# Optimization experiments

Hardware: AMD Instinct MI355X
Metric: run time of the kernel (lower is better)

Reference implementation:

```python
import jax, jax.numpy as jnp
import numpy as np

N_PTS = 131072
K_POSE = 4
J = 24
P_NUM = 64
R_COMP = 32
POSE_DIM = 32
GRID = (512, 512, 128)
MAT_MODE = ((0, 1), (0, 2), (1, 2))


def sample_line(line, xs):
    # line: [k, R, G], xs: [N] in [-1, 1].
    # Equivalent to F.grid_sample on a [k,R,G,1] map with grid x-coord fixed to 0
    # (W==1 so the x dim is degenerate) -> 1D linear interpolation along G.
    G = line.shape[-1]
    pos = (xs + 1.0) * 0.5 * (G - 1)
    i0 = jnp.clip(jnp.floor(pos), 0, G - 1).astype(jnp.int32)
    i1 = jnp.clip(i0 + 1, 0, G - 1)
    w = pos - i0.astype(xs.dtype)
    v0 = jnp.take(line, i0, axis=-1)  # [k,R,N]
    v1 = jnp.take(line, i1, axis=-1)
    return v0 * (1.0 - w) + v1 * w


def blend(w, A):
    # w: [1,N,J], A: [1,J,4,4] -> per-point blended LBS transform [1,N,4,4]
    return jnp.einsum('bnj,bjuv->bnuv', w, A)


def lbs_points(pts, T, inverse):
    Rm = T[..., :3, :3]
    t = T[..., :3, 3]
    if inverse:
        return jnp.einsum('bnij,bnj->bni', jnp.linalg.inv(Rm), pts - t)
    return jnp.einsum('bnij,bnj->bni', Rm, pts) + t


def lbs_dirs(d, T, inverse):
    Rm = T[..., :3, :3]
    if inverse:
        return jnp.einsum('bnij,bnj->bni', jnp.linalg.inv(Rm), d)
    return jnp.einsum('bnij,bnj->bni', Rm, d)


def setup_inputs() -> dict:
    key = jax.random.key(0)
    ks = jax.random.split(key, 12)
    pose_pts = 0.3 * jax.random.normal(ks[0], (1, N_PTS, 3), jnp.float32)
    pose_dirs = jax.random.normal(ks[1], (1, N_PTS, 3), jnp.float32)
    sw = jax.random.uniform(ks[2], (1, N_PTS, J), dtype=jnp.float32)
    skinning_weight = sw / jnp.sum(sw, axis=-1, keepdims=True)
    eye = jnp.eye(4, dtype=jnp.float32)
    A = eye + 0.2 * jax.random.normal(ks[3], (1, J, 4, 4), jnp.float32)
    big_A = eye + 0.2 * jax.random.normal(ks[4], (1, J, 4, 4), jnp.float32)
    tbounds = jnp.array([[-1.5, -1.5, -1.5], [1.5, 1.5, 1.5]], jnp.float32)
    coord_line0 = 0.1 * jax.random.normal(ks[5], (P_NUM, R_COMP, GRID[0], 1), jnp.float32)
    coord_line1 = 0.1 * jax.random.normal(ks[6], (P_NUM, R_COMP, GRID[1], 1), jnp.float32)
    coord_line2 = 0.1 * jax.random.normal(ks[7], (P_NUM, R_COMP, GRID[2], 1), jnp.float32)
    feat_line0 = 0.1 * jax.random.normal(ks[8], (P_NUM, R_COMP, POSE_DIM, 1), jnp.float32)
    feat_line1 = 0.1 * jax.random.normal(ks[9], (P_NUM, R_COMP, POSE_DIM, 1), jnp.float32)
    feat_line2 = 0.1 * jax.random.normal(ks[10], (P_NUM, R_COMP, POSE_DIM, 1), jnp.float32)
    tw = jax.random.uniform(ks[11], (K_POSE,), dtype=jnp.float32) + 0.1
    topk_weight = tw / jnp.sum(tw)  # L1-normalized top-k pose weights
    topk_id = jax.random.randint(jax.random.fold_in(key, 7), (K_POSE,), 0, P_NUM, dtype=jnp.int32)
    return dict(pose_pts=pose_pts, pose_dirs=pose_dirs, skinning_weight=skinning_weight,
                A=A, big_A=big_A, tbounds=tbounds,
                coord_line0=coord_line0, coord_line1=coord_line1, coord_line2=coord_line2,
                feat_line0=feat_line0, feat_line1=feat_line1, feat_line2=feat_line2,
                topk_weight=topk_weight, topk_id=topk_id)


def reference(pose_pts, pose_dirs, skinning_weight, A, big_A, tbounds,
              coord_line0, coord_line1, coord_line2,
              feat_line0, feat_line1, feat_line2,
              topk_weight, topk_id):
    # --- backward_deform: observed pose -> t-pose (inv A) -> big/canonical pose (big_A) ---
    T_A = blend(skinning_weight, A)
    T_big = blend(skinning_weight, big_A)
    tpose = lbs_points(pose_pts, T_A, inverse=True)
    cnl_pts = lbs_points(tpose, T_big, inverse=False)   # [1,N,3]
    tdirs = lbs_dirs(pose_dirs, T_A, inverse=True)
    cnl_dirs = lbs_dirs(tdirs, T_big, inverse=False)    # [1,N,3]
    # --- get_pose_feat: normalize_pts detaches pts, then TensoRF-style line sampling ---
    npts = jax.lax.stop_gradient(cnl_pts)
    npts = (npts - tbounds[0]) / (tbounds[1] - tbounds[0]) * 2.0 - 1.0  # [1,N,3]
    coord_lines = (coord_line0, coord_line1, coord_line2)
    feat_lines = (feat_line0, feat_line1, feat_line2)
    coords, feats = [], []
    for i in range(3):
        line = coord_lines[i][topk_id][..., 0]           # [k,R,G_i]
        coords.append(sample_line(line, npts[0, :, i]))  # [k,R,N]
        feats.append(feat_lines[i][topk_id][..., 0])     # [k,R,C]
    planes = []
    for p, (i0, i1) in enumerate(MAT_MODE):
        t = coords[i0] * coords[i1]                      # [k,R,N] outer-product term
        planes.append(jnp.einsum('krn,krc->knc', t, feats[p]))  # reduce over R
    pose_feats = jnp.concatenate(planes, axis=-1)        # [k,N,3C]
    pose_feat = jnp.sum(topk_weight[:, None, None] * pose_feats, axis=0, keepdims=True)
    return jnp.concatenate([cnl_pts, cnl_dirs, pose_feat], axis=-1)  # [1,N,102]
```

## Files before the change

kernel.cpp:

```cpp
#include <hip/hip_runtime.h>

#define NPTS 131072
#define G0 512
#define G1 512
#define G2 128

#define SKIN_BLOCKS  512
#define TRANS_BLOCKS 576
#define FEAT_BLOCKS  48

#define OFF1 (4*G0*32)
#define OFF2 (4*(G0+G1)*32)
#define LTOT (4*(G0+G1+G2)*32)

typedef float v4f __attribute__((ext_vector_type(4)));
typedef __attribute__((ext_vector_type(8))) short short8;

__device__ unsigned short g_lines16[LTOT + 32];
__device__ unsigned short g_featB[3*4*2*64*8];
__device__ float4 g_pos[NPTS];

__device__ __forceinline__ unsigned short bf16rne(float x){
  unsigned int u = __float_as_uint(x);
  u += 0x7fffu + ((u >> 16) & 1u);
  return (unsigned short)(u >> 16);
}

__device__ __forceinline__ void cvt8(uint4 r, float* f){
  f[0] = __uint_as_float(r.x << 16); f[1] = __uint_as_float(r.x & 0xffff0000u);
  f[2] = __uint_as_float(r.y << 16); f[3] = __uint_as_float(r.y & 0xffff0000u);
  f[4] = __uint_as_float(r.z << 16); f[5] = __uint_as_float(r.z & 0xffff0000u);
  f[6] = __uint_as_float(r.w << 16); f[7] = __uint_as_float(r.w & 0xffff0000u);
}

__device__ __forceinline__ void lerp_rows(const unsigned short* p, float w, float* c){
  uint4 r0 = *(const uint4*)p;
  uint4 r1 = *(const uint4*)(p + 32);
  float a[8], b[8];
  cvt8(r0, a); cvt8(r1, b);
  #pragma unroll
  for (int j = 0; j < 8; j++) c[j] = fmaf(w, b[j] - a[j], a[j]);
}

__device__ __forceinline__ unsigned int pack2(float lo, float hi){
  unsigned int ul = __float_as_uint(lo) + 0x8000u;
  unsigned int uh = __float_as_uint(hi) + 0x8000u;
  return __builtin_amdgcn_perm(uh, ul, 0x07060302u);
}

__global__ __launch_bounds__(256) void prep_skin(
    const float* __restrict__ pts, const float* __restrict__ dirs,
    const float* __restrict__ sw,  const float* __restrict__ Am,
    const float* __restrict__ Bm,  const float* __restrict__ tb,
    const float* __restrict__ c0,  const float* __restrict__ c1,
    const float* __restrict__ c2,  const float* __restrict__ f0,
    const float* __restrict__ f1,  const float* __restrict__ f2,
    const float* __restrict__ tw,  const int* __restrict__ topk_id,
    float* __restrict__ out)
{
  const int bid = blockIdx.x;
  const int tid = threadIdx.x;

  if (bid >= SKIN_BLOCKS) {
    int pb = bid - SKIN_BLOCKS;
    if (pb < TRANS_BLOCKS) {
      int e = pb*256 + tid;
      const float* src; int logG, outoff;
      if (e < 65536)       { src = c0; logG = 9; outoff = 0; }
      else if (e < 131072) { e -= 65536;  src = c1; logG = 9; outoff = OFF1; }
      else                 { e -= 131072; src = c2; logG = 7; outoff = OFF2; }
      const int G = 1 << logG;
      int g  = e & (G-1);
      int t  = e >> logG;
      int r  = t & 31;
      int kk = t >> 5;
      int id = topk_id[kk];
      float v = src[(id*32 + r)*G + g];
      g_lines16[outoff + (kk*G + g)*32 + r] = bf16rne(v);
    } else {
      int e = (pb - TRANS_BLOCKS)*256 + tid;
      if (e < 3*4*2*64*8) {
        int j    =  e        & 7;
        int lane = (e >> 3)  & 63;
        int tcol = (e >> 9)  & 1;
        int s    = (e >> 10) & 3;
        int p    =  e >> 12;
        int r = ((lane >> 4) << 3) + j;
        int cc = tcol*16 + (lane & 15);
        const float* f = (p == 0) ? f0 : ((p == 1) ? f1 : f2);
        float v = tw[s] * f[(topk_id[s]*32 + r)*32 + cc];
        g_featB[e] = bf16rne(v);
      }
    }
    return;
  }

  if (bid == 0 && tid < 32) g_lines16[LTOT + tid] = 0;

  __shared__ float sA[384];
  __shared__ float sB[384];
  for (int i = tid; i < 384; i += 256){ sA[i] = Am[i]; sB[i] = Bm[i]; }
  __syncthreads();

  const int n = bid*256 + tid;
  float swv[24];
  {
    const float4* swp = reinterpret_cast<const float4*>(sw + n*24);
    #pragma unroll
    for (int i = 0; i < 6; i++){
      float4 v = swp[i];
      swv[4*i] = v.x; swv[4*i+1] = v.y; swv[4*i+2] = v.z; swv[4*i+3] = v.w;
    }
  }
  float RA[9] = {0,0,0,0,0,0,0,0,0}, tA[3] = {0,0,0};
  float RB[9] = {0,0,0,0,0,0,0,0,0}, tB[3] = {0,0,0};
  #pragma unroll
  for (int j = 0; j < 24; j++){
    float w = swv[j];
    const float* a = sA + j*16;
    const float* b = sB + j*16;
    RA[0] = fmaf(w, a[0], RA[0]); RA[1] = fmaf(w, a[1], RA[1]); RA[2] = fmaf(w, a[2], RA[2]); tA[0] = fmaf(w, a[3],  tA[0]);
    RA[3] = fmaf(w, a[4], RA[3]); RA[4] = fmaf(w, a[5], RA[4]); RA[5] = fmaf(w, a[6], RA[5]); tA[1] = fmaf(w, a[7],  tA[1]);
    RA[6] = fmaf(w, a[8], RA[6]); RA[7] = fmaf(w, a[9], RA[7]); RA[8] = fmaf(w, a[10],RA[8]); tA[2] = fmaf(w, a[11], tA[2]);
    RB[0] = fmaf(w, b[0], RB[0]); RB[1] = fmaf(w, b[1], RB[1]); RB[2] = fmaf(w, b[2], RB[2]); tB[0] = fmaf(w, b[3],  tB[0]);
    RB[3] = fmaf(w, b[4], RB[3]); RB[4] = fmaf(w, b[5], RB[4]); RB[5] = fmaf(w, b[6], RB[5]); tB[1] = fmaf(w, b[7],  tB[1]);
    RB[6] = fmaf(w, b[8], RB[6]); RB[7] = fmaf(w, b[9], RB[7]); RB[8] = fmaf(w, b[10],RB[8]); tB[2] = fmaf(w, b[11], tB[2]);
  }
  float c00 = RA[4]*RA[8] - RA[5]*RA[7];
  float c01 = RA[5]*RA[6] - RA[3]*RA[8];
  float c02 = RA[3]*RA[7] - RA[4]*RA[6];
  float det = RA[0]*c00 + RA[1]*c01 + RA[2]*c02;
  float idet = 1.0f/det;
  float i00 = c00*idet;
  float i01 = (RA[2]*RA[7] - RA[1]*RA[8])*idet;
  float i02 = (RA[1]*RA[5] - RA[2]*RA[4])*idet;
  float i10 = c01*idet;
  float i11 = (RA[0]*RA[8] - RA[2]*RA[6])*idet;
  float i12 = (RA[2]*RA[3] - RA[0]*RA[5])*idet;
  float i20 = c02*idet;
  float i21 = (RA[1]*RA[6] - RA[0]*RA[7])*idet;
  float i22 = (RA[0]*RA[4] - RA[1]*RA[3])*idet;

  float px = pts[n*3+0], py = pts[n*3+1], pz = pts[n*3+2];
  float dx = dirs[n*3+0], dy = dirs[n*3+1], dz = dirs[n*3+2];
  float qx = px - tA[0], qy = py - tA[1], qz = pz - tA[2];
  float tpx = i00*qx + i01*qy + i02*qz;
  float tpy = i10*qx + i11*qy + i12*qz;
  float tpz = i20*qx + i21*qy + i22*qz;
  float cx = RB[0]*tpx + RB[1]*tpy + RB[2]*tpz + tB[0];
  float cy = RB[3]*tpx + RB[4]*tpy + RB[5]*tpz + tB[1];
  float cz = RB[6]*tpx + RB[7]*tpy + RB[8]*tpz + tB[2];
  float tdx = i00*dx + i01*dy + i02*dz;
  float tdy = i10*dx + i11*dy + i12*dz;
  float tdz = i20*dx + i21*dy + i22*dz;
  float cdx = RB[0]*tdx + RB[1]*tdy + RB[2]*tdz;
  float cdy = RB[3]*tdx + RB[4]*tdy + RB[5]*tdz;
  float cdz = RB[6]*tdx + RB[7]*tdy + RB[8]*tdz;

  {
    float* o = out + (size_t)n*102;
    o[0] = cx; o[1] = cy; o[2] = cz; o[3] = cdx; o[4] = cdy; o[5] = cdz;
  }
  {
    float lo0 = tb[0], lo1 = tb[1], lo2 = tb[2];
    float hi0 = tb[3], hi1 = tb[4], hi2 = tb[5];
    float x0 = (cx - lo0)/(hi0 - lo0)*2.0f - 1.0f;
    float x1 = (cy - lo1)/(hi1 - lo1)*2.0f - 1.0f;
    float x2 = (cz - lo2)/(hi2 - lo2)*2.0f - 1.0f;
    float4 p;
    p.x = (x0 + 1.0f)*0.5f*(float)(G0-1);
    p.y = (x1 + 1.0f)*0.5f*(float)(G1-1);
    p.z = (x2 + 1.0f)*0.5f*(float)(G2-1);
    p.w = 0.0f;
    g_pos[n] = p;
  }
}

__global__ __launch_bounds__(256) void einsum_mfma(float* __restrict__ out)
{
  const int tid  = threadIdx.x;
  const int lane = tid & 63;
  const int wv   = tid >> 6;
  const int m    = lane & 15;
  const int q    = lane >> 4;
  const int tile = blockIdx.x*4 + wv;
  const int pl   = tile*16 + m;

  float4 pos = g_pos[pl];
  float pc0 = fminf(fmaxf(pos.x, 0.0f), (float)(G0-1));
  float pc1 = fminf(fmaxf(pos.y, 0.0f), (float)(G1-1));
  float pc2 = fminf(fmaxf(pos.z, 0.0f), (float)(G2-1));
  float fl0 = floorf(pc0), fl1 = floorf(pc1), fl2 = floorf(pc2);
  int a0 = (int)fl0, a1 = (int)fl1, a2 = (int)fl2;
  float w0 = pc0 - fl0, w1 = pc1 - fl1, w2 = pc2 - fl2;

  const unsigned short* lt0 = g_lines16;
  const unsigned short* lt1 = g_lines16 + OFF1;
  const unsigned short* lt2 = g_lines16 + OFF2;
  const short8* fb = reinterpret_cast<const short8*>(g_featB);

  v4f acc00 = {0,0,0,0}, acc01 = {0,0,0,0};
  v4f acc10 = {0,0,0,0}, acc11 = {0,0,0,0};
  v4f acc20 = {0,0,0,0}, acc21 = {0,0,0,0};

  #pragma unroll
  for (int s = 0; s < 4; s++){
    float c0[8], c1[8], c2[8];
    lerp_rows(lt0 + (s*G0 + a0)*32 + q*8, w0, c0);
    lerp_rows(lt1 + (s*G1 + a1)*32 + q*8, w1, c1);
    lerp_rows(lt2 + (s*G2 + a2)*32 + q*8, w2, c2);

    uint4 A0u, A1u, A2u;
    A0u.x = pack2(c0[0]*c1[0], c0[1]*c1[1]);
    A0u.y = pack2(c0[2]*c1[2], c0[3]*c1[3]);
    A0u.z = pack2(c0[4]*c1[4], c0[5]*c1[5]);
    A0u.w = pack2(c0[6]*c1[6], c0[7]*c1[7]);
    A1u.x = pack2(c0[0]*c2[0], c0[1]*c2[1]);
    A1u.y = pack2(c0[2]*c2[2], c0[3]*c2[3]);
    A1u.z = pack2(c0[4]*c2[4], c0[5]*c2[5]);
    A1u.w = pack2(c0[6]*c2[6], c0[7]*c2[7]);
    A2u.x = pack2(c1[0]*c2[0], c1[1]*c2[1]);
    A2u.y = pack2(c1[2]*c2[2], c1[3]*c2[3]);
    A2u.z = pack2(c1[4]*c2[4], c1[5]*c2[5]);
    A2u.w = pack2(c1[6]*c2[6], c1[7]*c2[7]);
    short8 A0 = __builtin_bit_cast(short8, A0u);
    short8 A1 = __builtin_bit_cast(short8, A1u);
    short8 A2 = __builtin_bit_cast(short8, A2u);

    short8 B00 = fb[(0*8 + s*2 + 0)*64 + lane];
    short8 B01 = fb[(0*8 + s*2 + 1)*64 + lane];
    short8 B10 = fb[(1*8 + s*2 + 0)*64 + lane];
    short8 B11 = fb[(1*8 + s*2 + 1)*64 + lane];
    short8 B20 = fb[(2*8 + s*2 + 0)*64 + lane];
    short8 B21 = fb[(2*8 + s*2 + 1)*64 + lane];
    acc00 = __builtin_amdgcn_mfma_f32_16x16x32_bf16(A0, B00, acc00, 0, 0, 0);
    acc01 = __builtin_amdgcn_mfma_f32_16x16x32_bf16(A0, B01, acc01, 0, 0, 0);
    acc10 = __builtin_amdgcn_mfma_f32_16x16x32_bf16(A1, B10, acc10, 0, 0, 0);
    acc11 = __builtin_amdgcn_mfma_f32_16x16x32_bf16(A1, B11, acc11, 0, 0, 0);
    acc20 = __builtin_amdgcn_mfma_f32_16x16x32_bf16(A2, B20, acc20, 0, 0, 0);
    acc21 = __builtin_amdgcn_mfma_f32_16x16x32_bf16(A2, B21, acc21, 0, 0, 0);
  }

  const int rowBase = tile*16 + q*4;
  #pragma unroll
  for (int v = 0; v < 4; v++){
    float* o = out + (size_t)(rowBase + v)*102 + 6 + m;
    o[0]  = acc00[v];
    o[16] = acc01[v];
    o[32] = acc10[v];
    o[48] = acc11[v];
    o[64] = acc20[v];
    o[80] = acc21[v];
  }
}

extern "C" void kernel_launch(void* const* d_in, const int* in_sizes, int n_in,
                              void* d_out, int out_size, void* d_ws, size_t ws_size,
                              hipStream_t stream) {
  const float* pose_pts  = (const float*)d_in[0];
  const float* pose_dirs = (const float*)d_in[1];
  const float* sw        = (const float*)d_in[2];
  const float* Am        = (const float*)d_in[3];
  const float* Bm        = (const float*)d_in[4];
  const float* tb        = (const float*)d_in[5];
  const float* cl0       = (const float*)d_in[6];
  const float* cl1       = (const float*)d_in[7];
  const float* cl2       = (const float*)d_in[8];
  const float* fl0       = (const float*)d_in[9];
  const float* fl1       = (const float*)d_in[10];
  const float* fl2       = (const float*)d_in[11];
  const float* tw        = (const float*)d_in[12];
  const int*   tkid      = (const int*)d_in[13];
  float* out = (float*)d_out;

  hipLaunchKernelGGL(prep_skin, dim3(SKIN_BLOCKS + TRANS_BLOCKS + FEAT_BLOCKS), dim3(256), 0, stream,
                     pose_pts, pose_dirs, sw, Am, Bm, tb,
                     cl0, cl1, cl2, fl0, fl1, fl2, tw, tkid, out);
  hipLaunchKernelGGL(einsum_mfma, dim3(NPTS/(4*16)), dim3(256), 0, stream, out);
}
```

Before: 137.0 us.

## Process two point tiles per wave, vectorize line transpose and skin output stores

The einsum kernel now handles two 16-point tiles per wave. It issues all six gathered line-row loads for both tiles before the lerp and MFMA work, and reuses each B fragment load across both tiles, which halves the grid. The line transpose in the prep kernel now packs four bf16 values per thread into an 8-byte store, cutting its block count by four. The six leading output floats are written as three float2 stores. The cost is higher register pressure from twelve accumulators and buffered loads, which may reduce occupancy.

```diff
diff --git a/kernel.cpp b/kernel.cpp
--- a/kernel.cpp
+++ b/kernel.cpp
@@ -6,7 +6,7 @@
 #define G2 128
 
 #define SKIN_BLOCKS  512
-#define TRANS_BLOCKS 576
+#define TRANS_BLOCKS 144
 #define FEAT_BLOCKS  48
 
 #define OFF1 (4*G0*32)
@@ -33,9 +33,7 @@
   f[6] = __uint_as_float(r.w << 16); f[7] = __uint_as_float(r.w & 0xffff0000u);
 }
 
-__device__ __forceinline__ void lerp_rows(const unsigned short* p, float w, float* c){
-  uint4 r0 = *(const uint4*)p;
-  uint4 r1 = *(const uint4*)(p + 32);
+__device__ __forceinline__ void lerp_regs(uint4 r0, uint4 r1, float w, float* c){
   float a[8], b[8];
   cvt8(r0, a); cvt8(r1, b);
   #pragma unroll
@@ -66,17 +64,24 @@
     if (pb < TRANS_BLOCKS) {
       int e = pb*256 + tid;
       const float* src; int logG, outoff;
-      if (e < 65536)       { src = c0; logG = 9; outoff = 0; }
-      else if (e < 131072) { e -= 65536;  src = c1; logG = 9; outoff = OFF1; }
-      else                 { e -= 131072; src = c2; logG = 7; outoff = OFF2; }
+      if (e < 16384)      { src = c0; logG = 9; outoff = 0; }
+      else if (e < 32768) { e -= 16384; src = c1; logG = 9; outoff = OFF1; }
+      else                { e -= 32768; src = c2; logG = 7; outoff = OFF2; }
       const int G = 1 << logG;
       int g  = e & (G-1);
       int t  = e >> logG;
-      int r  = t & 31;
-      int kk = t >> 5;
+      int r4 = t & 7;
+      int kk = t >> 3;
       int id = topk_id[kk];
-      float v = src[(id*32 + r)*G + g];
-      g_lines16[outoff + (kk*G + g)*32 + r] = bf16rne(v);
+      const float* s0 = src + (id*32 + r4*4)*G + g;
+      float v0 = s0[0];
+      float v1 = s0[G];
+      float v2 = s0[2*G];
+      float v3 = s0[3*G];
+      unsigned int lo = ((unsigned int)bf16rne(v0)) | (((unsigned int)bf16rne(v1)) << 16);
+      unsigned int hi = ((unsigned int)bf16rne(v2)) | (((unsigned int)bf16rne(v3)) << 16);
+      uint2 w; w.x = lo; w.y = hi;
+      *reinterpret_cast<uint2*>(&g_lines16[outoff + (kk*G + g)*32 + r4*4]) = w;
     } else {
       int e = (pb - TRANS_BLOCKS)*256 + tid;
       if (e < 3*4*2*64*8) {
@@ -158,8 +163,11 @@
   float cdz = RB[6]*tdx + RB[7]*tdy + RB[8]*tdz;
 
   {
-    float* o = out + (size_t)n*102;
-    o[0] = cx; o[1] = cy; o[2] = cz; o[3] = cdx; o[4] = cdy; o[5] = cdz;
+    float2* o2 = reinterpret_cast<float2*>(out + (size_t)n*102);
+    float2 a; a.x = cx;  a.y = cy;
+    float2 b; b.x = cz;  b.y = cdx;
+    float2 c; c.x = cdy; c.y = cdz;
+    o2[0] = a; o2[1] = b; o2[2] = c;
   }
   {
     float lo0 = tb[0], lo1 = tb[1], lo2 = tb[2];
@@ -183,74 +191,98 @@
   const int wv   = tid >> 6;
   const int m    = lane & 15;
   const int q    = lane >> 4;
-  const int tile = blockIdx.x*4 + wv;
-  const int pl   = tile*16 + m;
-
-  float4 pos = g_pos[pl];
-  float pc0 = fminf(fmaxf(pos.x, 0.0f), (float)(G0-1));
-  float pc1 = fminf(fmaxf(pos.y, 0.0f), (float)(G1-1));
-  float pc2 = fminf(fmaxf(pos.z, 0.0f), (float)(G2-1));
-  float fl0 = floorf(pc0), fl1 = floorf(pc1), fl2 = floorf(pc2);
-  int a0 = (int)fl0, a1 = (int)fl1, a2 = (int)fl2;
-  float w0 = pc0 - fl0, w1 = pc1 - fl1, w2 = pc2 - fl2;
+  const int tileBase = (blockIdx.x*4 + wv)*2;
 
   const unsigned short* lt0 = g_lines16;
   const unsigned short* lt1 = g_lines16 + OFF1;
   const unsigned short* lt2 = g_lines16 + OFF2;
   const short8* fb = reinterpret_cast<const short8*>(g_featB);
 
-  v4f acc00 = {0,0,0,0}, acc01 = {0,0,0,0};
-  v4f acc10 = {0,0,0,0}, acc11 = {0,0,0,0};
-  v4f acc20 = {0,0,0,0}, acc21 = {0,0,0,0};
+  int a0[2], a1[2], a2[2];
+  float w0[2], w1[2], w2[2];
+  #pragma unroll
+  for (int i = 0; i < 2; i++){
+    float4 pos = g_pos[(tileBase + i)*16 + m];
+    float pc0 = fminf(fmaxf(pos.x, 0.0f), (float)(G0-1));
+    float pc1 = fminf(fmaxf(pos.y, 0.0f), (float)(G1-1));
+    float pc2 = fminf(fmaxf(pos.z, 0.0f), (float)(G2-1));
+    float fl0 = floorf(pc0), fl1 = floorf(pc1), fl2 = floorf(pc2);
+    a0[i] = (int)fl0; a1[i] = (int)fl1; a2[i] = (int)fl2;
+    w0[i] = pc0 - fl0; w1[i] = pc1 - fl1; w2[i] = pc2 - fl2;
+  }
+
+  v4f acc[2][6];
+  #pragma unroll
+  for (int i = 0; i < 2; i++)
+    #pragma unroll
+    for (int p = 0; p < 6; p++) acc[i][p] = (v4f){0,0,0,0};
 
   #pragma unroll
   for (int s = 0; s < 4; s++){
-    float c0[8], c1[8], c2[8];
-    lerp_rows(lt0 + (s*G0 + a0)*32 + q*8, w0, c0);
-    lerp_rows(lt1 + (s*G1 + a1)*32 + q*8, w1, c1);
-    lerp_rows(lt2 + (s*G2 + a2)*32 + q*8, w2, c2);
-
-    uint4 A0u, A1u, A2u;
-    A0u.x = pack2(c0[0]*c1[0], c0[1]*c1[1]);
-    A0u.y = pack2(c0[2]*c1[2], c0[3]*c1[3]);
-    A0u.z = pack2(c0[4]*c1[4], c0[5]*c1[5]);
-    A0u.w = pack2(c0[6]*c1[6], c0[7]*c1[7]);
-    A1u.x = pack2(c0[0]*c2[0], c0[1]*c2[1]);
-    A1u.y = pack2(c0[2]*c2[2], c0[3]*c2[3]);
-    A1u.z = pack2(c0[4]*c2[4], c0[5]*c2[5]);
-    A1u.w = pack2(c0[6]*c2[6], c0[7]*c2[7]);
-    A2u.x = pack2(c1[0]*c2[0], c1[1]*c2[1]);
-    A2u.y = pack2(c1[2]*c2[2], c1[3]*c2[3]);
-    A2u.z = pack2(c1[4]*c2[4], c1[5]*c2[5]);
-    A2u.w = pack2(c1[6]*c2[6], c1[7]*c2[7]);
-    short8 A0 = __builtin_bit_cast(short8, A0u);
-    short8 A1 = __builtin_bit_cast(short8, A1u);
-    short8 A2 = __builtin_bit_cast(short8, A2u);
-
     short8 B00 = fb[(0*8 + s*2 + 0)*64 + lane];
     short8 B01 = fb[(0*8 + s*2 + 1)*64 + lane];
     short8 B10 = fb[(1*8 + s*2 + 0)*64 + lane];
     short8 B11 = fb[(1*8 + s*2 + 1)*64 + lane];
     short8 B20 = fb[(2*8 + s*2 + 0)*64 + lane];
     short8 B21 = fb[(2*8 + s*2 + 1)*64 + lane];
-    acc00 = __builtin_amdgcn_mfma_f32_16x16x32_bf16(A0, B00, acc00, 0, 0, 0);
-    acc01 = __builtin_amdgcn_mfma_f32_16x16x32_bf16(A0, B01, acc01, 0, 0, 0);
-    acc10 = __builtin_amdgcn_mfma_f32_16x16x32_bf16(A1, B10, acc10, 0, 0, 0);
-    acc11 = __builtin_amdgcn_mfma_f32_16x16x32_bf16(A1, B11, acc11, 0, 0, 0);
-    acc20 = __builtin_amdgcn_mfma_f32_16x16x32_bf16(A2, B20, acc20, 0, 0, 0);
-    acc21 = __builtin_amdgcn_mfma_f32_16x16x32_bf16(A2, B21, acc21, 0, 0, 0);
-  }
-
-  const int rowBase = tile*16 + q*4;
-  #pragma unroll
-  for (int v = 0; v < 4; v++){
-    float* o = out + (size_t)(rowBase + v)*102 + 6 + m;
-    o[0]  = acc00[v];
-    o[16] = acc01[v];
-    o[32] = acc10[v];
-    o[48] = acc11[v];
-    o[64] = acc20[v];
-    o[80] = acc21[v];
+
+    uint4 r0a[2], r1a[2], r0b[2], r1b[2], r0c[2], r1c[2];
+    #pragma unroll
+    for (int i = 0; i < 2; i++){
+      const unsigned short* p0 = lt0 + (s*G0 + a0[i])*32 + q*8;
+      r0a[i] = *(const uint4*)p0;  r1a[i] = *(const uint4*)(p0 + 32);
+      const unsigned short* p1 = lt1 + (s*G1 + a1[i])*32 + q*8;
+      r0b[i] = *(const uint4*)p1;  r1b[i] = *(const uint4*)(p1 + 32);
+      const unsigned short* p2 = lt2 + (s*G2 + a2[i])*32 + q*8;
+      r0c[i] = *(const uint4*)p2;  r1c[i] = *(const uint4*)(p2 + 32);
+    }
+
+    #pragma unroll
+    for (int i = 0; i < 2; i++){
+      float c0[8], c1[8], c2[8];
+      lerp_regs(r0a[i], r1a[i], w0[i], c0);
+      lerp_regs(r0b[i], r1b[i], w1[i], c1);
+      lerp_regs(r0c[i], r1c[i], w2[i], c2);
+
+      uint4 A0u, A1u, A2u;
+      A0u.x = pack2(c0[0]*c1[0], c0[1]*c1[1]);
+      A0u.y = pack2(c0[2]*c1[2], c0[3]*c1[3]);
+      A0u.z = pack2(c0[4]*c1[4], c0[5]*c1[5]);
+      A0u.w = pack2(c0[6]*c1[6], c0[7]*c1[7]);
+      A1u.x = pack2(c0[0]*c2[0], c0[1]*c2[1]);
+      A1u.y = pack2(c0[2]*c2[2], c0[3]*c2[3]);
+      A1u.z = pack2(c0[4]*c2[4], c0[5]*c2[5]);
+      A1u.w = pack2(c0[6]*c2[6], c0[7]*c2[7]);
+      A2u.x = pack2(c1[0]*c2[0], c1[1]*c2[1]);
+      A2u.y = pack2(c1[2]*c2[2], c1[3]*c2[3]);
+      A2u.z = pack2(c1[4]*c2[4], c1[5]*c2[5]);
+      A2u.w = pack2(c1[6]*c2[6], c1[7]*c2[7]);
+      short8 A0 = __builtin_bit_cast(short8, A0u);
+      short8 A1 = __builtin_bit_cast(short8, A1u);
+      short8 A2 = __builtin_bit_cast(short8, A2u);
+
+      acc[i][0] = __builtin_amdgcn_mfma_f32_16x16x32_bf16(A0, B00, acc[i][0], 0, 0, 0);
+      acc[i][1] = __builtin_amdgcn_mfma_f32_16x16x32_bf16(A0, B01, acc[i][1], 0, 0, 0);
+      acc[i][2] = __builtin_amdgcn_mfma_f32_16x16x32_bf16(A1, B10, acc[i][2], 0, 0, 0);
+      acc[i][3] = __builtin_amdgcn_mfma_f32_16x16x32_bf16(A1, B11, acc[i][3], 0, 0, 0);
+      acc[i][4] = __builtin_amdgcn_mfma_f32_16x16x32_bf16(A2, B20, acc[i][4], 0, 0, 0);
+      acc[i][5] = __builtin_amdgcn_mfma_f32_16x16x32_bf16(A2, B21, acc[i][5], 0, 0, 0);
+    }
+  }
+
+  #pragma unroll
+  for (int i = 0; i < 2; i++){
+    const int rowBase = (tileBase + i)*16 + q*4;
+    #pragma unroll
+    for (int v = 0; v < 4; v++){
+      float* o = out + (size_t)(rowBase + v)*102 + 6 + m;
+      o[0]  = acc[i][0][v];
+      o[16] = acc[i][1][v];
+      o[32] = acc[i][2][v];
+      o[48] = acc[i][3][v];
+      o[64] = acc[i][4][v];
+      o[80] = acc[i][5][v];
+    }
   }
 }
 
@@ -276,5 +308,5 @@
   hipLaunchKernelGGL(prep_skin, dim3(SKIN_BLOCKS + TRANS_BLOCKS + FEAT_BLOCKS), dim3(256), 0, stream,
                      pose_pts, pose_dirs, sw, Am, Bm, tb,
                      cl0, cl1, cl2, fl0, fl1, fl2, tw, tkid, out);
-  hipLaunchKernelGGL(einsum_mfma, dim3(NPTS/(4*16)), dim3(256), 0, stream, out);
-}
+  hipLaunchKernelGGL(einsum_mfma, dim3(NPTS/(8*16)), dim3(256), 0, stream, out);
+}
```

Measured after the change: 136.0 us. No clear change (-0.7%).

## Fuse skinning with MFMA einsum and split small line/feature prep kernel

Applied to the files above, without the earlier changes.

The per-point skinning stage now feeds the MFMA einsum directly inside one kernel. Positions pass through shared memory instead of a global g_pos buffer, and the bf16 feature matrix is staged into LDS per block. Line transposition moves to its own small kernel that writes four bf16 values per thread, and the first six outputs are written as float2 stores. The aim is to remove the global round trip for positions and give the point-wise work the whole grid. The trade-off is fewer blocks (512) each doing four tiles serially with more LDS, which may reduce latency hiding.

```diff
diff --git a/kernel.cpp b/kernel.cpp
--- a/kernel.cpp
+++ b/kernel.cpp
@@ -5,20 +5,18 @@
 #define G1 512
 #define G2 128
 
-#define SKIN_BLOCKS  512
-#define TRANS_BLOCKS 576
-#define FEAT_BLOCKS  48
-
 #define OFF1 (4*G0*32)
 #define OFF2 (4*(G0+G1)*32)
 #define LTOT (4*(G0+G1+G2)*32)
 
+#define TRANS_BLOCKS 144
+#define FEAT_BLOCKS  48
+
 typedef float v4f __attribute__((ext_vector_type(4)));
 typedef __attribute__((ext_vector_type(8))) short short8;
 
 __device__ unsigned short g_lines16[LTOT + 32];
 __device__ unsigned short g_featB[3*4*2*64*8];
-__device__ float4 g_pos[NPTS];
 
 __device__ __forceinline__ unsigned short bf16rne(float x){
   unsigned int u = __float_as_uint(x);
@@ -33,9 +31,7 @@
   f[6] = __uint_as_float(r.w << 16); f[7] = __uint_as_float(r.w & 0xffff0000u);
 }
 
-__device__ __forceinline__ void lerp_rows(const unsigned short* p, float w, float* c){
-  uint4 r0 = *(const uint4*)p;
-  uint4 r1 = *(const uint4*)(p + 32);
+__device__ __forceinline__ void lerp_regs(uint4 r0, uint4 r1, float w, float* c){
   float a[8], b[8];
   cvt8(r0, a); cvt8(r1, b);
   #pragma unroll
@@ -48,61 +44,76 @@
   return __builtin_amdgcn_perm(uh, ul, 0x07060302u);
 }
 
-__global__ __launch_bounds__(256) void prep_skin(
+__global__ __launch_bounds__(256) void prep_small(
+    const float* __restrict__ c0,  const float* __restrict__ c1,
+    const float* __restrict__ c2,  const float* __restrict__ f0,
+    const float* __restrict__ f1,  const float* __restrict__ f2,
+    const float* __restrict__ tw,  const int* __restrict__ topk_id)
+{
+  const int bid = blockIdx.x;
+  const int tid = threadIdx.x;
+  if (bid == 0 && tid < 32) g_lines16[LTOT + tid] = 0;
+
+  if (bid < TRANS_BLOCKS) {
+    int e = bid*256 + tid;
+    const float* src; int logG, outoff;
+    if (e < 16384)      { src = c0; logG = 9; outoff = 0; }
+    else if (e < 32768) { e -= 16384; src = c1; logG = 9; outoff = OFF1; }
+    else                { e -= 32768; src = c2; logG = 7; outoff = OFF2; }
+    const int G = 1 << logG;
+    int g  = e & (G-1);
+    int t  = e >> logG;
+    int r4 = t & 7;
+    int kk = t >> 3;
+    int id = topk_id[kk];
+    const float* s0 = src + (id*32 + r4*4)*G + g;
+    float v0 = s0[0];
+    float v1 = s0[G];
+    float v2 = s0[2*G];
+    float v3 = s0[3*G];
+    unsigned int lo = ((unsigned int)bf16rne(v0)) | (((unsigned int)bf16rne(v1)) << 16);
+    unsigned int hi = ((unsigned int)bf16rne(v2)) | (((unsigned int)bf16rne(v3)) << 16);
+    uint2 w; w.x = lo; w.y = hi;
+    *reinterpret_cast<uint2*>(&g_lines16[outoff + (kk*G + g)*32 + r4*4]) = w;
+  } else {
+    int e = (bid - TRANS_BLOCKS)*256 + tid;
+    if (e < 3*4*2*64*8) {
+      int j    =  e        & 7;
+      int lane = (e >> 3)  & 63;
+      int tcol = (e >> 9)  & 1;
+      int s    = (e >> 10) & 3;
+      int p    =  e >> 12;
+      int r = ((lane >> 4) << 3) + j;
+      int cc = tcol*16 + (lane & 15);
+      const float* f = (p == 0) ? f0 : ((p == 1) ? f1 : f2);
+      float v = tw[s] * f[(topk_id[s]*32 + r)*32 + cc];
+      g_featB[e] = bf16rne(v);
+    }
+  }
+}
+
+__global__ __launch_bounds__(256) void fused_main(
     const float* __restrict__ pts, const float* __restrict__ dirs,
     const float* __restrict__ sw,  const float* __restrict__ Am,
     const float* __restrict__ Bm,  const float* __restrict__ tb,
-    const float* __restrict__ c0,  const float* __restrict__ c1,
-    const float* __restrict__ c2,  const float* __restrict__ f0,
-    const float* __restrict__ f1,  const float* __restrict__ f2,
-    const float* __restrict__ tw,  const int* __restrict__ topk_id,
     float* __restrict__ out)
 {
-  const int bid = blockIdx.x;
-  const int tid = threadIdx.x;
-
-  if (bid >= SKIN_BLOCKS) {
-    int pb = bid - SKIN_BLOCKS;
-    if (pb < TRANS_BLOCKS) {
-      int e = pb*256 + tid;
-      const float* src; int logG, outoff;
-      if (e < 65536)       { src = c0; logG = 9; outoff = 0; }
-      else if (e < 131072) { e -= 65536;  src = c1; logG = 9; outoff = OFF1; }
-      else                 { e -= 131072; src = c2; logG = 7; outoff = OFF2; }
-      const int G = 1 << logG;
-      int g  = e & (G-1);
-      int t  = e >> logG;
-      int r  = t & 31;
-      int kk = t >> 5;
-      int id = topk_id[kk];
-      float v = src[(id*32 + r)*G + g];
-      g_lines16[outoff + (kk*G + g)*32 + r] = bf16rne(v);
-    } else {
-      int e = (pb - TRANS_BLOCKS)*256 + tid;
-      if (e < 3*4*2*64*8) {
-        int j    =  e        & 7;
-        int lane = (e >> 3)  & 63;
-        int tcol = (e >> 9)  & 1;
-        int s    = (e >> 10) & 3;
-        int p    =  e >> 12;
-        int r = ((lane >> 4) << 3) + j;
-        int cc = tcol*16 + (lane & 15);
-        const float* f = (p == 0) ? f0 : ((p == 1) ? f1 : f2);
-        float v = tw[s] * f[(topk_id[s]*32 + r)*32 + cc];
-        g_featB[e] = bf16rne(v);
-      }
-    }
-    return;
-  }
-
-  if (bid == 0 && tid < 32) g_lines16[LTOT + tid] = 0;
-
   __shared__ float sA[384];
   __shared__ float sB[384];
+  __shared__ unsigned short sFeat[3*4*2*64*8];
+  __shared__ float4 sPos[256];
+
+  const int tid = threadIdx.x;
+
   for (int i = tid; i < 384; i += 256){ sA[i] = Am[i]; sB[i] = Bm[i]; }
+  {
+    const uint4* gs = reinterpret_cast<const uint4*>(g_featB);
+    uint4* gd = reinterpret_cast<uint4*>(sFeat);
+    for (int i = tid; i < (3*4*2*64*8)/8; i += 256) gd[i] = gs[i];
+  }
   __syncthreads();
 
-  const int n = bid*256 + tid;
+  const int n = blockIdx.x*256 + tid;
   float swv[24];
   {
     const float4* swp = reinterpret_cast<const float4*>(sw + n*24);
@@ -158,8 +169,11 @@
   float cdz = RB[6]*tdx + RB[7]*tdy + RB[8]*tdz;
 
   {
-    float* o = out + (size_t)n*102;
-    o[0] = cx; o[1] = cy; o[2] = cz; o[3] = cdx; o[4] = cdy; o[5] = cdz;
+    float2* o2 = reinterpret_cast<float2*>(out + (size_t)n*102);
+    float2 a; a.x = cx;  a.y = cy;
+    float2 b; b.x = cz;  b.y = cdx;
+    float2 c; c.x = cdy; c.y = cdz;
+    o2[0] = a; o2[1] = b; o2[2] = c;
   }
   {
     float lo0 = tb[0], lo1 = tb[1], lo2 = tb[2];
@@ -172,85 +186,90 @@
     p.y = (x1 + 1.0f)*0.5f*(float)(G1-1);
     p.z = (x2 + 1.0f)*0.5f*(float)(G2-1);
     p.w = 0.0f;
-    g_pos[n] = p;
-  }
-}
-
-__global__ __launch_bounds__(256) void einsum_mfma(float* __restrict__ out)
-{
-  const int tid  = threadIdx.x;
+    sPos[tid] = p;
+  }
+  __syncthreads();
+
   const int lane = tid & 63;
   const int wv   = tid >> 6;
   const int m    = lane & 15;
   const int q    = lane >> 4;
-  const int tile = blockIdx.x*4 + wv;
-  const int pl   = tile*16 + m;
-
-  float4 pos = g_pos[pl];
-  float pc0 = fminf(fmaxf(pos.x, 0.0f), (float)(G0-1));
-  float pc1 = fminf(fmaxf(pos.y, 0.0f), (float)(G1-1));
-  float pc2 = fminf(fmaxf(pos.z, 0.0f), (float)(G2-1));
-  float fl0 = floorf(pc0), fl1 = floorf(pc1), fl2 = floorf(pc2);
-  int a0 = (int)fl0, a1 = (int)fl1, a2 = (int)fl2;
-  float w0 = pc0 - fl0, w1 = pc1 - fl1, w2 = pc2 - fl2;
-
   const unsigned short* lt0 = g_lines16;
   const unsigned short* lt1 = g_lines16 + OFF1;
   const unsigned short* lt2 = g_lines16 + OFF2;
-  const short8* fb = reinterpret_cast<const short8*>(g_featB);
-
-  v4f acc00 = {0,0,0,0}, acc01 = {0,0,0,0};
-  v4f acc10 = {0,0,0,0}, acc11 = {0,0,0,0};
-  v4f acc20 = {0,0,0,0}, acc21 = {0,0,0,0};
-
-  #pragma unroll
-  for (int s = 0; s < 4; s++){
-    float c0[8], c1[8], c2[8];
-    lerp_rows(lt0 + (s*G0 + a0)*32 + q*8, w0, c0);
-    lerp_rows(lt1 + (s*G1 + a1)*32 + q*8, w1, c1);
-    lerp_rows(lt2 + (s*G2 + a2)*32 + q*8, w2, c2);
-
-    uint4 A0u, A1u, A2u;
-    A0u.x = pack2(c0[0]*c1[0], c0[1]*c1[1]);
-    A0u.y = pack2(c0[2]*c1[2], c0[3]*c1[3]);
-    A0u.z = pack2(c0[4]*c1[4], c0[5]*c1[5]);
-    A0u.w = pack2(c0[6]*c1[6], c0[7]*c1[7]);
-    A1u.x = pack2(c0[0]*c2[0], c0[1]*c2[1]);
-    A1u.y = pack2(c0[2]*c2[2], c0[3]*c2[3]);
-    A1u.z = pack2(c0[4]*c2[4], c0[5]*c2[5]);
-    A1u.w = pack2(c0[6]*c2[6], c0[7]*c2[7]);
-    A2u.x = pack2(c1[0]*c2[0], c1[1]*c2[1]);
-    A2u.y = pack2(c1[2]*c2[2], c1[3]*c2[3]);
-    A2u.z = pack2(c1[4]*c2[4], c1[5]*c2[5]);
-    A2u.w = pack2(c1[6]*c2[6], c1[7]*c2[7]);
-    short8 A0 = __builtin_bit_cast(short8, A0u);
-    short8 A1 = __builtin_bit_cast(short8, A1u);
-    short8 A2 = __builtin_bit_cast(short8, A2u);
-
-    short8 B00 = fb[(0*8 + s*2 + 0)*64 + lane];
-    short8 B01 = fb[(0*8 + s*2 + 1)*64 + lane];
-    short8 B10 = fb[(1*8 + s*2 + 0)*64 + lane];
-    short8 B11 = fb[(1*8 + s*2 + 1)*64 + lane];
-    short8 B20 = fb[(2*8 + s*2 + 0)*64 + lane];
-    short8 B21 = fb[(2*8 + s*2 + 1)*64 + lane];
-    acc00 = __builtin_amdgcn_mfma_f32_16x16x32_bf16(A0, B00, acc00, 0, 0, 0);
-    acc01 = __builtin_amdgcn_mfma_f32_16x16x32_bf16(A0, B01, acc01, 0, 0, 0);
-    acc10 = __builtin_amdgcn_mfma_f32_16x16x32_bf16(A1, B10, acc10, 0, 0, 0);
-    acc11 = __builtin_amdgcn_mfma_f32_16x16x32_bf16(A1, B11, acc11, 0, 0, 0);
-    acc20 = __builtin_amdgcn_mfma_f32_16x16x32_bf16(A2, B20, acc20, 0, 0, 0);
-    acc21 = __builtin_amdgcn_mfma_f32_16x16x32_bf16(A2, B21, acc21, 0, 0, 0);
-  }
-
-  const int rowBase = tile*16 + q*4;
-  #pragma unroll
-  for (int v = 0; v < 4; v++){
-    float* o = out + (size_t)(rowBase + v)*102 + 6 + m;
-    o[0]  = acc00[v];
-    o[16] = acc01[v];
-    o[32] = acc10[v];
-    o[48] = acc11[v];
-    o[64] = acc20[v];
-    o[80] = acc21[v];
+  const short8* fb = reinterpret_cast<const short8*>(sFeat);
+
+  for (int t = 0; t < 4; t++){
+    const int pl = wv*64 + t*16 + m;
+    float4 pos = sPos[pl];
+    float pc0 = fminf(fmaxf(pos.x, 0.0f), (float)(G0-1));
+    float pc1 = fminf(fmaxf(pos.y, 0.0f), (float)(G1-1));
+    float pc2 = fminf(fmaxf(pos.z, 0.0f), (float)(G2-1));
+    float fl0 = floorf(pc0), fl1 = floorf(pc1), fl2 = floorf(pc2);
+    int a0 = (int)fl0, a1 = (int)fl1, a2 = (int)fl2;
+    float w0 = pc0 - fl0, w1 = pc1 - fl1, w2 = pc2 - fl2;
+
+    v4f acc00 = {0,0,0,0}, acc01 = {0,0,0,0};
+    v4f acc10 = {0,0,0,0}, acc11 = {0,0,0,0};
+    v4f acc20 = {0,0,0,0}, acc21 = {0,0,0,0};
+
+    #pragma unroll
+    for (int s = 0; s < 4; s++){
+      const unsigned short* p0 = lt0 + (s*G0 + a0)*32 + q*8;
+      uint4 r0a = *(const uint4*)p0;  uint4 r1a = *(const uint4*)(p0 + 32);
+      const unsigned short* p1 = lt1 + (s*G1 + a1)*32 + q*8;
+      uint4 r0b = *(const uint4*)p1;  uint4 r1b = *(const uint4*)(p1 + 32);
+      const unsigned short* p2 = lt2 + (s*G2 + a2)*32 + q*8;
+      uint4 r0c = *(const uint4*)p2;  uint4 r1c = *(const uint4*)(p2 + 32);
+
+      short8 B00 = fb[(0*8 + s*2 + 0)*64 + lane];
+      short8 B01 = fb[(0*8 + s*2 + 1)*64 + lane];
+      short8 B10 = fb[(1*8 + s*2 + 0)*64 + lane];
+      short8 B11 = fb[(1*8 + s*2 + 1)*64 + lane];
+      short8 B20 = fb[(2*8 + s*2 + 0)*64 + lane];
+      short8 B21 = fb[(2*8 + s*2 + 1)*64 + lane];
+
+      float c0[8], c1[8], c2[8];
+      lerp_regs(r0a, r1a, w0, c0);
+      lerp_regs(r0b, r1b, w1, c1);
+      lerp_regs(r0c, r1c, w2, c2);
+
+      uint4 A0u, A1u, A2u;
+      A0u.x = pack2(c0[0]*c1[0], c0[1]*c1[1]);
+      A0u.y = pack2(c0[2]*c1[2], c0[3]*c1[3]);
+      A0u.z = pack2(c0[4]*c1[4], c0[5]*c1[5]);
+      A0u.w = pack2(c0[6]*c1[6], c0[7]*c1[7]);
+      A1u.x = pack2(c0[0]*c2[0], c0[1]*c2[1]);
+      A1u.y = pack2(c0[2]*c2[2], c0[3]*c2[3]);
+      A1u.z = pack2(c0[4]*c2[4], c0[5]*c2[5]);
+      A1u.w = pack2(c0[6]*c2[6], c0[7]*c2[7]);
+      A2u.x = pack2(c1[0]*c2[0], c1[1]*c2[1]);
+      A2u.y = pack2(c1[2]*c2[2], c1[3]*c2[3]);
+      A2u.z = pack2(c1[4]*c2[4], c1[5]*c2[5]);
+      A2u.w = pack2(c1[6]*c2[6], c1[7]*c2[7]);
+      short8 A0 = __builtin_bit_cast(short8, A0u);
+      short8 A1 = __builtin_bit_cast(short8, A1u);
+      short8 A2 = __builtin_bit_cast(short8, A2u);
+
+      acc00 = __builtin_amdgcn_mfma_f32_16x16x32_bf16(A0, B00, acc00, 0, 0, 0);
+      acc01 = __builtin_amdgcn_mfma_f32_16x16x32_bf16(A0, B01, acc01, 0, 0, 0);
+      acc10 = __builtin_amdgcn_mfma_f32_16x16x32_bf16(A1, B10, acc10, 0, 0, 0);
+      acc11 = __builtin_amdgcn_mfma_f32_16x16x32_bf16(A1, B11, acc11, 0, 0, 0);
+      acc20 = __builtin_amdgcn_mfma_f32_16x16x32_bf16(A2, B20, acc20, 0, 0, 0);
+      acc21 = __builtin_amdgcn_mfma_f32_16x16x32_bf16(A2, B21, acc21, 0, 0, 0);
+    }
+
+    const int rowBase = blockIdx.x*256 + wv*64 + t*16 + q*4;
+    #pragma unroll
+    for (int v = 0; v < 4; v++){
+      float* o = out + (size_t)(rowBase + v)*102 + 6 + m;
+      o[0]  = acc00[v];
+      o[16] = acc01[v];
+      o[32] = acc10[v];
+      o[48] = acc11[v];
+      o[64] = acc20[v];
+      o[80] = acc21[v];
+    }
   }
 }
 
@@ -273,8 +292,8 @@
   const int*   tkid      = (const int*)d_in[13];
   float* out = (float*)d_out;
 
-  hipLaunchKernelGGL(prep_skin, dim3(SKIN_BLOCKS + TRANS_BLOCKS + FEAT_BLOCKS), dim3(256), 0, stream,
-                     pose_pts, pose_dirs, sw, Am, Bm, tb,
-                     cl0, cl1, cl2, fl0, fl1, fl2, tw, tkid, out);
-  hipLaunchKernelGGL(einsum_mfma, dim3(NPTS/(4*16)), dim3(256), 0, stream, out);
-}
+  hipLaunchKernelGGL(prep_small, dim3(TRANS_BLOCKS + FEAT_BLOCKS), dim3(256), 0, stream,
+                     cl0, cl1, cl2, fl0, fl1, fl2, tw, tkid);
+  hipLaunchKernelGGL(fused_main, dim3(NPTS/256), dim3(256), 0, stream,
+                     pose_pts, pose_dirs, sw, Am, Bm, tb, out);
+}
```

New measurement: 144.8 us. 1.06x slower.
